# Optimization experiments

Hardware: AMD Instinct MI355X
Metric: run time of the kernel (lower is better)

Reference implementation:

```python
import jax, jax.numpy as jnp
import numpy as np

H = 128
N = 100000
E = 1000000
IN_DIM = 2 * H + 2


def setup_inputs() -> dict:
    key = jax.random.key(0)
    ks = jax.random.split(key, 10)
    node_embed = jax.random.normal(ks[0], (N, H), dtype=jnp.float32)
    edge_index_score = jax.random.randint(ks[1], (2, E), 0, N, dtype=jnp.int64)
    edge_attr_score = jax.random.uniform(ks[2], (E, 2), dtype=jnp.float32)
    # MLP params (kaiming-ish scale)
    W1 = jax.random.normal(ks[3], (IN_DIM, H), dtype=jnp.float32) / np.sqrt(IN_DIM)
    b1 = jnp.zeros((H,), dtype=jnp.float32)
    ln_gamma = jnp.ones((H,), dtype=jnp.float32)
    ln_beta = jnp.zeros((H,), dtype=jnp.float32)
    W2 = jax.random.normal(ks[4], (H, H // 2), dtype=jnp.float32) / np.sqrt(H)
    b2 = jnp.zeros((H // 2,), dtype=jnp.float32)
    W3 = jax.random.normal(ks[5], (H // 2, 1), dtype=jnp.float32) / np.sqrt(H // 2)
    b3 = jnp.zeros((1,), dtype=jnp.float32)
    return {
        "node_embed": node_embed,
        "edge_index_score": edge_index_score,
        "edge_attr_score": edge_attr_score,
        "W1": W1, "b1": b1, "ln_gamma": ln_gamma, "ln_beta": ln_beta,
        "W2": W2, "b2": b2, "W3": W3, "b3": b3,
    }


def _layernorm(x, gamma, beta, eps=1e-5):
    mu = jnp.mean(x, axis=-1, keepdims=True)
    var = jnp.mean(jnp.square(x - mu), axis=-1, keepdims=True)
    return (x - mu) * jax.lax.rsqrt(var + eps) * gamma + beta


def reference(node_embed, edge_index_score, edge_attr_score,
              W1, b1, ln_gamma, ln_beta, W2, b2, W3, b3):
    i_idx = edge_index_score[0]
    j_idx = edge_index_score[1]
    # [E, 2H+2]
    e_in = jnp.concatenate([node_embed[i_idx], node_embed[j_idx], edge_attr_score], axis=-1)
    h = _layernorm(e_in @ W1 + b1, ln_gamma, ln_beta)
    h = jax.nn.relu(h)  # dropout is identity in eval mode
    h = jax.nn.relu(h @ W2 + b2)
    logit = h @ W3 + b3
    return logit.squeeze(-1)  # [E]
```

## Files before the change

### kernel.cpp

```cpp
#include <hip/hip_runtime.h>
#include <hip/hip_bf16.h>
#include <hip/hip_fp16.h>

typedef __attribute__((ext_vector_type(8))) short short8;
typedef __attribute__((ext_vector_type(4))) float f32x4;
typedef unsigned short ushort_t;

namespace {

constexpr int H     = 128;
constexpr int E     = 1000000;
constexpr int NNODE = 100000;
constexpr int EB    = 512;
constexpr int NTILE = (E + EB - 1) / EB;
constexpr int GRID  = 256;
constexpr int TPB   = NTILE / GRID;
constexpr int REM   = NTILE - TPB * GRID;

constexpr size_t AT_OFF  = 0;
constexpr size_t AT_SZ   = (size_t)NNODE * 256 * 2;
constexpr size_t W1F_OFF = AT_SZ;
constexpr size_t W1F_SZ  = 64 * 64 * 8 * 2;
constexpr size_t W2F_OFF = W1F_OFF + W1F_SZ;
constexpr size_t W2F_SZ  = 20 * 64 * 8 * 2;
constexpr size_t WS_NEED = W2F_OFF + W2F_SZ;

__device__ __forceinline__ ushort_t f2bf(float x) {
    unsigned u = __float_as_uint(x);
    return (ushort_t)((u + 0x7FFFu + ((u >> 16) & 1u)) >> 16);
}
__device__ __forceinline__ unsigned pkbf(float a, float b) {
    __hip_bfloat162 t = __float22bfloat162_rn(make_float2(a, b));
    return *reinterpret_cast<unsigned*>(&t);
}
__device__ __forceinline__ unsigned pkhf(float a, float b) {
    __half2 t = __float22half2_rn(make_float2(a, b));
    return *reinterpret_cast<unsigned*>(&t);
}
__device__ __forceinline__ int imin(int a, int b) { return a < b ? a : b; }

union FragU { int4 i; short8 s; };
union HalfU { short8 s; __half h[8]; };

typedef const __attribute__((address_space(1))) unsigned int* gptr_t;
typedef __attribute__((address_space(3))) unsigned int* lptr_t;

__device__ __forceinline__ void gload16(const void* g, void* l) {
    __builtin_amdgcn_global_load_lds((gptr_t)g, (lptr_t)l, 16, 0, 0);
}

__global__ void cvt_wfrag(const float* __restrict__ W1, const float* __restrict__ W2,
                          const float* __restrict__ b2,
                          ushort_t* __restrict__ w1f, ushort_t* __restrict__ w2f) {
    int u = blockIdx.x, l = threadIdx.x;
    int lo = l & 15, hi = l >> 4;
    if (u < 64) {
        int s = u >> 3, n = u & 7, col = n * 16 + lo;
#pragma unroll
        for (int j = 0; j < 8; ++j) {
            int kk = s * 32 + hi * 8 + j;
            w1f[(u * 64 + l) * 8 + j] = f2bf(W1[kk * 128 + col]);
        }
    } else {
        int u2 = u - 64;
        int s = u2 >> 2, n = u2 & 3, col = n * 16 + lo;
#pragma unroll
        for (int j = 0; j < 8; ++j) {
            int kk = s * 32 + hi * 8 + j;
            float v = (kk < 128) ? W2[kk * 64 + col]
                    : (kk == 128 ? b2[col] : 0.f);
            w2f[(u2 * 64 + l) * 8 + j] = f2bf(v);
        }
    }
}

struct PrepSm { ushort_t w1f[32768]; };

__global__ __launch_bounds__(512, 2)
void build_atab(const float* __restrict__ ne, const ushort_t* __restrict__ w1fg,
                const float* __restrict__ b1, ushort_t* __restrict__ atab) {
    __shared__ PrepSm sm;
    const int tid = threadIdx.x;
    {
        const uint4* s1 = reinterpret_cast<const uint4*>(w1fg);
        uint4*       d1 = reinterpret_cast<uint4*>(sm.w1f);
#pragma unroll
        for (int i = 0; i < 8; ++i) d1[i * 512 + tid] = s1[i * 512 + tid];
    }
    __syncthreads();

    const int wid = tid >> 6, lane = tid & 63;
    const int lo = lane & 15, hi = lane >> 4;
    const int nbase = blockIdx.x * 512 + wid * 64;
    const f32x4 z4 = {0.f, 0.f, 0.f, 0.f};

    short8 nf[4][4];
#pragma unroll
    for (int mt = 0; mt < 4; ++mt) {
        int node = imin(nbase + mt * 16 + lo, NNODE - 1);
        const float* row = ne + (size_t)node * H;
#pragma unroll
        for (int s = 0; s < 4; ++s) {
            f32x4 a = *reinterpret_cast<const f32x4*>(row + s * 32 + hi * 8);
            f32x4 b = *reinterpret_cast<const f32x4*>(row + s * 32 + hi * 8 + 4);
            FragU f;
            f.i = make_int4((int)pkbf(a[0], a[1]), (int)pkbf(a[2], a[3]),
                            (int)pkbf(b[0], b[1]), (int)pkbf(b[2], b[3]));
            nf[mt][s] = f.s;
        }
    }

#pragma unroll
    for (int X = 0; X < 2; ++X) {
        f32x4 acc[4][8];
        if (X == 0) {
#pragma unroll
            for (int n = 0; n < 8; ++n) {
                f32x4 b1v = *reinterpret_cast<const f32x4*>(b1 + n * 16 + hi * 4);
#pragma unroll
                for (int mt = 0; mt < 4; ++mt) acc[mt][n] = b1v;
            }
        } else {
#pragma unroll
            for (int mt = 0; mt < 4; ++mt)
#pragma unroll
                for (int n = 0; n < 8; ++n) acc[mt][n] = z4;
        }
#pragma unroll
        for (int s = 0; s < 4; ++s)
#pragma unroll
            for (int n = 0; n < 8; ++n) {
                short8 wa = *reinterpret_cast<const short8*>(
                    sm.w1f + (((X * 4 + s) * 8 + n) * 64 + lane) * 8);
#pragma unroll
                for (int mt = 0; mt < 4; ++mt)
                    acc[mt][n] = __builtin_amdgcn_mfma_f32_16x16x32_bf16(wa, nf[mt][s], acc[mt][n], 0, 0, 0);
            }
#pragma unroll
        for (int mt = 0; mt < 4; ++mt) {
            int node = nbase + mt * 16 + lo;
            if (node < NNODE) {
                ushort_t* dst = atab + (size_t)node * 256 + X * 128;
#pragma unroll
                for (int n = 0; n < 8; ++n) {
                    uint2 v = make_uint2(pkhf(acc[mt][n][0], acc[mt][n][1]),
                                         pkhf(acc[mt][n][2], acc[mt][n][3]));
                    *reinterpret_cast<uint2*>(dst + n * 16 + hi * 4) = v;
                }
            }
        }
    }
}

struct __align__(16) SmemT {
    char     gbuf[8][2][8192];
    ushort_t w2f[10240];
    float t0s[128], t1s[128], gs[128], bs[128], w3s[64];
};

#define GISSUE(slotp, iv, jv)                                                   \
    {                                                                           \
        const ushort_t* gi_ = atab + (size_t)(iv) * 256 + hi * 8;               \
        const ushort_t* gj_ = atab + (size_t)(jv) * 256 + 128 + hi * 8;         \
        char* lb_ = (slotp);                                                    \
        _Pragma("unroll")                                                       \
        for (int s_ = 0; s_ < 4; ++s_) gload16(gi_ + s_ * 32, lb_ + s_ * 1024); \
        _Pragma("unroll")                                                       \
        for (int s_ = 0; s_ < 4; ++s_) gload16(gj_ + s_ * 32, lb_ + 4096 + s_ * 1024); \
    }

#define SUBTILE(MT, slotp, WAITLIT, IV, JV)                                     \
    {                                                                           \
        asm volatile("s_waitcnt " WAITLIT ::: "memory");                        \
        __builtin_amdgcn_sched_barrier(0);                                      \
        float s1 = 0.f, s2v = 0.f;                                              \
        float x[4][8];                                                          \
        _Pragma("unroll")                                                       \
        for (int s = 0; s < 4; ++s) {                                           \
            HalfU ui, uj;                                                       \
            ui.s = *reinterpret_cast<const short8*>((slotp) + s * 1024 + lane * 16);        \
            uj.s = *reinterpret_cast<const short8*>((slotp) + 4096 + s * 1024 + lane * 16); \
            f32x4 t0a = *reinterpret_cast<const f32x4*>(sm.t0s + s * 32 + hi * 8);     \
            f32x4 t0b = *reinterpret_cast<const f32x4*>(sm.t0s + s * 32 + hi * 8 + 4); \
            f32x4 t1a = *reinterpret_cast<const f32x4*>(sm.t1s + s * 32 + hi * 8);     \
            f32x4 t1b = *reinterpret_cast<const f32x4*>(sm.t1s + s * 32 + hi * 8 + 4); \
            _Pragma("unroll")                                                   \
            for (int q = 0; q < 2; ++q) {                                       \
                f32x4 w0 = q ? t0b : t0a;                                       \
                f32x4 w1 = q ? t1b : t1a;                                       \
                _Pragma("unroll")                                               \
                for (int r = 0; r < 4; ++r) {                                   \
                    float t = __half2float(ui.h[q * 4 + r]) + __half2float(uj.h[q * 4 + r]); \
                    t = fmaf(av[MT].x, w0[r], t);                               \
                    t = fmaf(av[MT].y, w1[r], t);                               \
                    s1 += t; s2v = fmaf(t, t, s2v);                             \
                    x[s][q * 4 + r] = t;                                        \
                }                                                               \
            }                                                                   \
        }                                                                       \
                  \
        asm volatile("s_waitcnt lgkmcnt(0)" ::: "memory");                      \
        __builtin_amdgcn_sched_barrier(0);                                      \
        GISSUE(slotp, IV, JV);                                                  \
        __builtin_amdgcn_sched_barrier(0);                                      \
        s1 += __shfl_xor(s1, 16); s1 += __shfl_xor(s1, 32);                     \
        s2v += __shfl_xor(s2v, 16); s2v += __shfl_xor(s2v, 32);                 \
        float mean = s1 * (1.f / 128.f);                                        \
        float var  = s2v * (1.f / 128.f) - mean * mean;                         \
        float rstd = rsqrtf(var + 1e-5f);                                       \
        short8 hfr[4];                                                          \
        _Pragma("unroll")                                                       \
        for (int s = 0; s < 4; ++s) {                                           \
            f32x4 ga = *reinterpret_cast<const f32x4*>(sm.gs + s * 32 + hi * 8);     \
            f32x4 gb = *reinterpret_cast<const f32x4*>(sm.gs + s * 32 + hi * 8 + 4); \
            f32x4 ba = *reinterpret_cast<const f32x4*>(sm.bs + s * 32 + hi * 8);     \
            f32x4 bb = *reinterpret_cast<const f32x4*>(sm.bs + s * 32 + hi * 8 + 4); \
            float hv[8];                                                        \
            _Pragma("unroll")                                                   \
            for (int q = 0; q < 2; ++q) {                                       \
                f32x4 g = q ? gb : ga;                                          \
                f32x4 b = q ? bb : ba;                                          \
                _Pragma("unroll")                                               \
                for (int r = 0; r < 4; ++r)                                     \
                    hv[q * 4 + r] = fmaxf(                                      \
                        fmaf((x[s][q * 4 + r] - mean) * rstd, g[r], b[r]), 0.f);\
            }                                                                   \
            FragU f;                                                            \
            f.i = make_int4((int)pkbf(hv[0], hv[1]), (int)pkbf(hv[2], hv[3]),   \
                            (int)pkbf(hv[4], hv[5]), (int)pkbf(hv[6], hv[7]));  \
            hfr[s] = f.s;                                                       \
        }                                                                       \
        f32x4 a2[4];                                                            \
        _Pragma("unroll")                                                       \
        for (int n2 = 0; n2 < 4; ++n2) a2[n2] = zero4;                          \
        __builtin_amdgcn_s_setprio(1);                                          \
        _Pragma("unroll")                                                       \
        for (int s = 0; s < 4; ++s) {                                           \
            _Pragma("unroll")                                                   \
            for (int n2 = 0; n2 < 4; ++n2) {                                    \
                short8 wa = *reinterpret_cast<const short8*>(sm.w2f + ((s * 4 + n2) * 64 + lane) * 8); \
                a2[n2] = __builtin_amdgcn_mfma_f32_16x16x32_bf16(wa, hfr[s], a2[n2], 0, 0, 0); \
            }                                                                   \
        }                                                                       \
        {                                                                       \
            FragU cf; cf.i = make_int4(hi == 0 ? 0x3F80 : 0, 0, 0, 0);          \
            _Pragma("unroll")                                                   \
            for (int n2 = 0; n2 < 4; ++n2) {                                    \
                short8 wa = *reinterpret_cast<const short8*>(sm.w2f + ((16 + n2) * 64 + lane) * 8); \
                a2[n2] = __builtin_amdgcn_mfma_f32_16x16x32_bf16(wa, cf.s, a2[n2], 0, 0, 0);   \
            }                                                                   \
        }                                                                       \
        __builtin_amdgcn_s_setprio(0);                                          \
        float part = 0.f;                                                       \
        _Pragma("unroll")                                                       \
        for (int n2 = 0; n2 < 4; ++n2) {                                        \
            f32x4 w3v = *reinterpret_cast<const f32x4*>(sm.w3s + n2 * 16 + hi * 4); \
            _Pragma("unroll")                                                   \
            for (int r = 0; r < 4; ++r)                                         \
                part = fmaf(fmaxf(a2[n2][r], 0.f), w3v[r], part);               \
        }                                                                       \
        part += __shfl_xor(part, 16);                                           \
        part += __shfl_xor(part, 32);                                           \
        if (hi == 0) {                                                          \
            int e = tb + (MT) * 16 + lo;                                        \
            if (e < E) out[e] = part + b3s;                                     \
        }                                                                       \
    }

__global__ __launch_bounds__(512, 2)
void edge_mlp_mfma(const ushort_t* __restrict__ atab,
                   const ushort_t* __restrict__ w2fg,
                   const int*      __restrict__ eidx,
                   const float*    __restrict__ attr,
                   const float*    __restrict__ W1,
                   const float*    __restrict__ gamma_,
                   const float*    __restrict__ beta_,
                   const float*    __restrict__ W3,
                   const float*    __restrict__ b3,
                   float*          __restrict__ out) {
    __shared__ SmemT sm;
    const int tid = threadIdx.x;
    const int bid = blockIdx.x;

    {
        const uint4* s2 = reinterpret_cast<const uint4*>(w2fg);
        uint4*       d2 = reinterpret_cast<uint4*>(sm.w2f);
        for (int i = tid; i < 1280; i += 512) d2[i] = s2[i];
    }
    if (tid < 128) {
        sm.t0s[tid] = W1[256 * 128 + tid];
        sm.t1s[tid] = W1[257 * 128 + tid];
        sm.gs[tid]  = gamma_[tid];
        sm.bs[tid]  = beta_[tid];
        if (tid < 64) sm.w3s[tid] = W3[tid];
    }
    __syncthreads();

    const int wid = tid >> 6;
    const int lane = tid & 63;
    const int lo = lane & 15, hi = lane >> 4;
    const int ebl = wid * 64;
    const int nk = (bid < REM) ? TPB + 1 : TPB;
    char* slot0 = sm.gbuf[wid][0];
    char* slot1 = sm.gbuf[wid][1];
    const float2* attr2 = reinterpret_cast<const float2*>(attr);
    const float b3s = b3[0];
    const f32x4 zero4 = {0.f, 0.f, 0.f, 0.f};

    int ci[4], cj[4], ni[4], nj[4];
    float2 av[4], avn[4];

    {
        int tb0 = bid * EB + ebl;
#pragma unroll
        for (int mt = 0; mt < 4; ++mt) {
            int e = imin(tb0 + mt * 16 + lo, E - 1);
            ci[mt] = eidx[e]; cj[mt] = eidx[E + e];
            av[mt] = attr2[e];
        }
    }
    GISSUE(slot0, ci[0], cj[0]);
    GISSUE(slot1, ci[1], cj[1]);
    {
        int tb1 = (bid + imin(1, nk - 1) * GRID) * EB + ebl;
#pragma unroll
        for (int mt = 0; mt < 4; ++mt) {
            int e = imin(tb1 + mt * 16 + lo, E - 1);
            ni[mt] = eidx[e]; nj[mt] = eidx[E + e];
            avn[mt] = attr2[e];
        }
    }

    for (int k = 0; k < nk; ++k) {
        const int tb = (bid + k * GRID) * EB + ebl;

        SUBTILE(0, slot0, "vmcnt(20)", ci[2], cj[2]);
        SUBTILE(1, slot1, "vmcnt(20)", ci[3], cj[3]);
        SUBTILE(2, slot0, "vmcnt(10)", ni[0], nj[0]);
        SUBTILE(3, slot1, "vmcnt(10)", ni[1], nj[1]);

#pragma unroll
        for (int mt = 0; mt < 4; ++mt) { ci[mt] = ni[mt]; cj[mt] = nj[mt]; av[mt] = avn[mt]; }
        {
            int t2 = imin(k + 2, nk - 1);
            int tb2 = (bid + t2 * GRID) * EB + ebl;
#pragma unroll
            for (int mt = 0; mt < 4; ++mt) {
                int e = imin(tb2 + mt * 16 + lo, E - 1);
                ni[mt] = eidx[e]; nj[mt] = eidx[E + e];
                avn[mt] = attr2[e];
            }
        }
    }
}

}

extern "C" void kernel_launch(void* const* d_in, const int* in_sizes, int n_in,
                              void* d_out, int out_size, void* d_ws, size_t ws_size,
                              hipStream_t stream) {
    const float* node_embed = (const float*)d_in[0];
    const int*   eidx       = (const int*)  d_in[1];
    const float* attr       = (const float*)d_in[2];
    const float* W1         = (const float*)d_in[3];
    const float* b1         = (const float*)d_in[4];
    const float* gamma      = (const float*)d_in[5];
    const float* beta       = (const float*)d_in[6];
    const float* W2         = (const float*)d_in[7];
    const float* b2         = (const float*)d_in[8];
    const float* W3         = (const float*)d_in[9];
    const float* b3         = (const float*)d_in[10];
    float* out = (float*)d_out;

    if (ws_size < WS_NEED) return;

    char* ws = (char*)d_ws;
    ushort_t* atab = (ushort_t*)(ws + AT_OFF);
    ushort_t* w1f  = (ushort_t*)(ws + W1F_OFF);
    ushort_t* w2f  = (ushort_t*)(ws + W2F_OFF);

    cvt_wfrag<<<84, 64, 0, stream>>>(W1, W2, b2, w1f, w2f);
    build_atab<<<(NNODE + 511) / 512, 512, 0, stream>>>(node_embed, w1f, b1, atab);
    edge_mlp_mfma<<<GRID, 512, 0, stream>>>(atab, w2f, eidx, attr, W1,
                                            gamma, beta, W3, b3, out);
}
```

Before: 123.7 us.

## Compute edge pre-activation and LayerNorm in packed fp16 and use fp16 MFMA

```diff
diff --git a/kernel.cpp b/kernel.cpp
--- a/kernel.cpp
+++ b/kernel.cpp
@@ -4,6 +4,8 @@
 
 typedef __attribute__((ext_vector_type(8))) short short8;
 typedef __attribute__((ext_vector_type(4))) float f32x4;
+typedef _Float16 h2v __attribute__((ext_vector_type(2)));
+typedef _Float16 h8v __attribute__((ext_vector_type(8)));
 typedef unsigned short ushort_t;
 
 namespace {
@@ -40,7 +42,9 @@
 __device__ __forceinline__ int imin(int a, int b) { return a < b ? a : b; }
 
 union FragU { int4 i; short8 s; };
-union HalfU { short8 s; __half h[8]; };
+union SlotU { short8 s; h2v h[4]; };
+union H8U   { h8v v; h2v h[4]; int4 i; };
+union U32H  { unsigned u; h2v h; };
 
 typedef const __attribute__((address_space(1))) unsigned int* gptr_t;
 typedef __attribute__((address_space(3))) unsigned int* lptr_t;
@@ -69,7 +73,8 @@
             int kk = s * 32 + hi * 8 + j;
             float v = (kk < 128) ? W2[kk * 64 + col]
                     : (kk == 128 ? b2[col] : 0.f);
-            w2f[(u2 * 64 + l) * 8 + j] = f2bf(v);
+            __half hh = __float2half_rn(v);
+            w2f[(u2 * 64 + l) * 8 + j] = *reinterpret_cast<ushort_t*>(&hh);
         }
     }
 }
@@ -155,7 +160,8 @@
 struct __align__(16) SmemT {
     char     gbuf[8][2][8192];
     ushort_t w2f[10240];
-    float t0s[128], t1s[128], gs[128], bs[128], w3s[64];
+    unsigned t0h[64], t1h[64], gh[64], bh[64];
+    float    w3s[64];
 };
 
 #define GISSUE(slotp, iv, jv)                                                   \
@@ -173,29 +179,31 @@
     {                                                                           \
         asm volatile("s_waitcnt " WAITLIT ::: "memory");                        \
         __builtin_amdgcn_sched_barrier(0);                                      \
+        const _Float16 axs = (_Float16)av[MT].x;                                \
+        const _Float16 ays = (_Float16)av[MT].y;                                \
+        const h2v ax2 = {axs, axs};                                             \
+        const h2v ay2 = {ays, ays};                                             \
         float s1 = 0.f, s2v = 0.f;                                              \
-        float x[4][8];                                                          \
+        h2v x2[4][4];                                                           \
         _Pragma("unroll")                                                       \
         for (int s = 0; s < 4; ++s) {                                           \
-            HalfU ui, uj;                                                       \
+            SlotU ui, uj;                                                       \
             ui.s = *reinterpret_cast<const short8*>((slotp) + s * 1024 + lane * 16);        \
             uj.s = *reinterpret_cast<const short8*>((slotp) + 4096 + s * 1024 + lane * 16); \
-            f32x4 t0a = *reinterpret_cast<const f32x4*>(sm.t0s + s * 32 + hi * 8);     \
-            f32x4 t0b = *reinterpret_cast<const f32x4*>(sm.t0s + s * 32 + hi * 8 + 4); \
-            f32x4 t1a = *reinterpret_cast<const f32x4*>(sm.t1s + s * 32 + hi * 8);     \
-            f32x4 t1b = *reinterpret_cast<const f32x4*>(sm.t1s + s * 32 + hi * 8 + 4); \
-            _Pragma("unroll")                                                   \
-            for (int q = 0; q < 2; ++q) {                                       \
-                f32x4 w0 = q ? t0b : t0a;                                       \
-                f32x4 w1 = q ? t1b : t1a;                                       \
-                _Pragma("unroll")                                               \
-                for (int r = 0; r < 4; ++r) {                                   \
-                    float t = __half2float(ui.h[q * 4 + r]) + __half2float(uj.h[q * 4 + r]); \
-                    t = fmaf(av[MT].x, w0[r], t);                               \
-                    t = fmaf(av[MT].y, w1[r], t);                               \
-                    s1 += t; s2v = fmaf(t, t, s2v);                             \
-                    x[s][q * 4 + r] = t;                                        \
-                }                                                               \
+            uint4 t0p = *reinterpret_cast<const uint4*>(sm.t0h + s * 16 + hi * 4); \
+            uint4 t1p = *reinterpret_cast<const uint4*>(sm.t1h + s * 16 + hi * 4); \
+            const unsigned t0a[4] = {t0p.x, t0p.y, t0p.z, t0p.w};               \
+            const unsigned t1a[4] = {t1p.x, t1p.y, t1p.z, t1p.w};               \
+            _Pragma("unroll")                                                   \
+            for (int p = 0; p < 4; ++p) {                                       \
+                U32H w0; w0.u = t0a[p];                                         \
+                U32H w1; w1.u = t1a[p];                                         \
+                h2v t = ui.h[p] + uj.h[p];                                      \
+                t = __builtin_elementwise_fma(ax2, w0.h, t);                    \
+                t = __builtin_elementwise_fma(ay2, w1.h, t);                    \
+                x2[s][p] = t;                                                   \
+                s1  = __builtin_amdgcn_fdot2(t, one2, s1, false);               \
+                s2v = __builtin_amdgcn_fdot2(t, t, s2v, false);                 \
             }                                                                   \
         }                                                                       \
                   \
@@ -208,27 +216,28 @@
         float mean = s1 * (1.f / 128.f);                                        \
         float var  = s2v * (1.f / 128.f) - mean * mean;                         \
         float rstd = rsqrtf(var + 1e-5f);                                       \
-        short8 hfr[4];                                                          \
+        const _Float16 rs_ = (_Float16)rstd;                                    \
+        const _Float16 cs_ = (_Float16)(-mean * rstd);                          \
+        const h2v rs2 = {rs_, rs_};                                             \
+        const h2v cs2 = {cs_, cs_};                                             \
+        h8v hfr[4];                                                             \
         _Pragma("unroll")                                                       \
         for (int s = 0; s < 4; ++s) {                                           \
-            f32x4 ga = *reinterpret_cast<const f32x4*>(sm.gs + s * 32 + hi * 8);     \
-            f32x4 gb = *reinterpret_cast<const f32x4*>(sm.gs + s * 32 + hi * 8 + 4); \
-            f32x4 ba = *reinterpret_cast<const f32x4*>(sm.bs + s * 32 + hi * 8);     \
-            f32x4 bb = *reinterpret_cast<const f32x4*>(sm.bs + s * 32 + hi * 8 + 4); \
-            float hv[8];                                                        \
-            _Pragma("unroll")                                                   \
-            for (int q = 0; q < 2; ++q) {                                       \
-                f32x4 g = q ? gb : ga;                                          \
-                f32x4 b = q ? bb : ba;                                          \
-                _Pragma("unroll")                                               \
-                for (int r = 0; r < 4; ++r)                                     \
-                    hv[q * 4 + r] = fmaxf(                                      \
-                        fmaf((x[s][q * 4 + r] - mean) * rstd, g[r], b[r]), 0.f);\
+            uint4 gp = *reinterpret_cast<const uint4*>(sm.gh + s * 16 + hi * 4); \
+            uint4 bp = *reinterpret_cast<const uint4*>(sm.bh + s * 16 + hi * 4); \
+            const unsigned ga[4] = {gp.x, gp.y, gp.z, gp.w};                    \
+            const unsigned ba[4] = {bp.x, bp.y, bp.z, bp.w};                    \
+            H8U f;                                                              \
+            _Pragma("unroll")                                                   \
+            for (int p = 0; p < 4; ++p) {                                       \
+                U32H g_; g_.u = ga[p];                                          \
+                U32H b_; b_.u = ba[p];                                          \
+                h2v t = __builtin_elementwise_fma(x2[s][p], rs2, cs2);          \
+                t = __builtin_elementwise_fma(t, g_.h, b_.h);                   \
+                t = __builtin_elementwise_max(t, zero2);                        \
+                f.h[p] = t;                                                     \
             }                                                                   \
-            FragU f;                                                            \
-            f.i = make_int4((int)pkbf(hv[0], hv[1]), (int)pkbf(hv[2], hv[3]),   \
-                            (int)pkbf(hv[4], hv[5]), (int)pkbf(hv[6], hv[7]));  \
-            hfr[s] = f.s;                                                       \
+            hfr[s] = f.v;                                                       \
         }                                                                       \
         f32x4 a2[4];                                                            \
         _Pragma("unroll")                                                       \
@@ -238,16 +247,16 @@
         for (int s = 0; s < 4; ++s) {                                           \
             _Pragma("unroll")                                                   \
             for (int n2 = 0; n2 < 4; ++n2) {                                    \
-                short8 wa = *reinterpret_cast<const short8*>(sm.w2f + ((s * 4 + n2) * 64 + lane) * 8); \
-                a2[n2] = __builtin_amdgcn_mfma_f32_16x16x32_bf16(wa, hfr[s], a2[n2], 0, 0, 0); \
+                h8v wa = *reinterpret_cast<const h8v*>(sm.w2f + ((s * 4 + n2) * 64 + lane) * 8); \
+                a2[n2] = __builtin_amdgcn_mfma_f32_16x16x32_f16(wa, hfr[s], a2[n2], 0, 0, 0); \
             }                                                                   \
         }                                                                       \
         {                                                                       \
-            FragU cf; cf.i = make_int4(hi == 0 ? 0x3F80 : 0, 0, 0, 0);          \
+            H8U cf; cf.i = make_int4(hi == 0 ? 0x00003C00 : 0, 0, 0, 0);        \
             _Pragma("unroll")                                                   \
             for (int n2 = 0; n2 < 4; ++n2) {                                    \
-                short8 wa = *reinterpret_cast<const short8*>(sm.w2f + ((16 + n2) * 64 + lane) * 8); \
-                a2[n2] = __builtin_amdgcn_mfma_f32_16x16x32_bf16(wa, cf.s, a2[n2], 0, 0, 0);   \
+                h8v wa = *reinterpret_cast<const h8v*>(sm.w2f + ((16 + n2) * 64 + lane) * 8); \
+                a2[n2] = __builtin_amdgcn_mfma_f32_16x16x32_f16(wa, cf.v, a2[n2], 0, 0, 0);   \
             }                                                                   \
         }                                                                       \
         __builtin_amdgcn_s_setprio(0);                                          \
@@ -287,12 +296,12 @@
         uint4*       d2 = reinterpret_cast<uint4*>(sm.w2f);
         for (int i = tid; i < 1280; i += 512) d2[i] = s2[i];
     }
-    if (tid < 128) {
-        sm.t0s[tid] = W1[256 * 128 + tid];
-        sm.t1s[tid] = W1[257 * 128 + tid];
-        sm.gs[tid]  = gamma_[tid];
-        sm.bs[tid]  = beta_[tid];
-        if (tid < 64) sm.w3s[tid] = W3[tid];
+    if (tid < 64) {
+        sm.t0h[tid] = pkhf(W1[256 * H + 2 * tid], W1[256 * H + 2 * tid + 1]);
+        sm.t1h[tid] = pkhf(W1[257 * H + 2 * tid], W1[257 * H + 2 * tid + 1]);
+        sm.gh[tid]  = pkhf(gamma_[2 * tid], gamma_[2 * tid + 1]);
+        sm.bh[tid]  = pkhf(beta_[2 * tid], beta_[2 * tid + 1]);
+        sm.w3s[tid] = W3[tid];
     }
     __syncthreads();
 
@@ -306,6 +315,8 @@
     const float2* attr2 = reinterpret_cast<const float2*>(attr);
     const float b3s = b3[0];
     const f32x4 zero4 = {0.f, 0.f, 0.f, 0.f};
+    const h2v one2  = {(_Float16)1.f, (_Float16)1.f};
+    const h2v zero2 = {(_Float16)0.f, (_Float16)0.f};
 
     int ci[4], cj[4], ni[4], nj[4];
     float2 av[4], avn[4];
```

Measured after the change: 117.4 us. -5.1%, faster.
